# Kernel tuning notes

Measured on AMD Instinct MI355X. Metric: run time of the kernel, lower is better.

## Reference

```python
import jax, jax.numpy as jnp
import numpy as np

D_MODEL = 64
D_K = 64
D_V = 64
N_HEADS = 4
D_FF = 64
D_HALF = 32  # d_model / 2 in the sca_* MLPs


def _layer_norm(x, eps=1e-5):
    m = jnp.mean(x, axis=-1, keepdims=True)
    v = jnp.var(x, axis=-1, keepdims=True)
    return (x - m) / jnp.sqrt(v + eps)


def _sca(u, w1, w2):
    # nn.Sequential(Linear(64,32), ReLU, Linear(32,1)), no bias
    return jax.nn.relu(u @ w1) @ w2  # [B,1,1]


def setup_inputs() -> dict:
    key = jax.random.key(0)
    ks = jax.random.split(key, 20)
    B, L = 128, 512

    def lin(k, fan_in, fan_out):
        bound = 1.0 / np.sqrt(fan_in)
        return jax.random.uniform(k, (fan_in, fan_out), jnp.float32, -bound, bound)

    inp = {
        "input": jax.random.normal(ks[0], (B, L, D_MODEL), jnp.float32),
        "attn_mask": jax.random.bernoulli(ks[1], 0.1, (B, L, L)),
        "input_u": jax.random.normal(ks[2], (B, 1, D_MODEL), jnp.float32),
        "W_Q": lin(ks[3], D_MODEL, N_HEADS * D_K),
        "W_K": lin(ks[4], D_MODEL, N_HEADS * D_K),
        "W_V": lin(ks[5], D_MODEL, N_HEADS * D_V),
        "U_Q": lin(ks[6], D_MODEL, D_K),
        "U_K": lin(ks[7], D_MODEL, D_K),
        "U_V": lin(ks[8], D_MODEL, D_V),
        "sq1": lin(ks[9], D_MODEL, D_HALF),
        "sq2": lin(ks[10], D_HALF, 1),
        "sk1": lin(ks[11], D_MODEL, D_HALF),
        "sk2": lin(ks[12], D_HALF, 1),
        "sv1": lin(ks[13], D_MODEL, D_HALF),
        "sv2": lin(ks[14], D_HALF, 1),
        "fc": lin(ks[15], N_HEADS * D_V, D_MODEL),
        "ff1": lin(ks[16], D_MODEL, D_FF),
        "ff2": lin(ks[17], D_FF, D_MODEL),
    }
    return inp


def reference(input, attn_mask, input_u, W_Q, W_K, W_V, U_Q, U_K, U_V,
              sq1, sq2, sk1, sk2, sv1, sv2, fc, ff1, ff2):
    B, L, _ = input.shape
    scale = 1.0 / np.sqrt(D_K).astype(np.float32)

    # multi-head projections: [B, H, L, d]
    Q = (input @ W_Q).reshape(B, L, N_HEADS, D_K).transpose(0, 2, 1, 3)
    K = (input @ W_K).reshape(B, L, N_HEADS, D_K).transpose(0, 2, 1, 3)
    V = (input @ W_V).reshape(B, L, N_HEADS, D_V).transpose(0, 2, 1, 3)

    # per-batch scalar gates from input_u: [B,1,1]
    s_q = _sca(input_u, sq1, sq2)
    s_k = _sca(input_u, sk1, sk2)
    s_v = _sca(input_u, sv1, sv2)

    # single-head u projections, gated; broadcast over heads later
    u_Q = (input @ U_Q) * s_q  # [B, L, d_k]
    u_K = (input @ U_K) * s_k  # [B, L, d_k]
    u_V = (input @ U_V) * s_v  # [B, L, d_v]

    scores = jnp.einsum('bhqd,bhkd->bhqk', Q, K) * scale
    scores = scores + (jnp.einsum('bqd,bkd->bqk', u_Q, u_K) * scale)[:, None]
    scores = jnp.where(attn_mask[:, None], jnp.float32(-1e9), scores)
    attn = jax.nn.softmax(scores, axis=-1)  # [B, H, L, L]

    context = jnp.einsum('bhqk,bhkd->bhqd', attn, V + u_V[:, None])
    context = context.transpose(0, 2, 1, 3).reshape(B, L, N_HEADS * D_V)

    out = context @ fc  # dropout is identity in eval
    enc = _layer_norm(out + input)

    # position-wise FFN with residual + layernorm
    ffn = jax.nn.relu(enc @ ff1) @ ff2
    enc_outputs = _layer_norm(ffn + enc)
    return (enc_outputs, attn)
```

## Files before the change

### kernel.cpp

```cpp
#include <hip/hip_runtime.h>

typedef unsigned char  u8;
typedef unsigned short u16;
typedef unsigned int   u32;

typedef __attribute__((ext_vector_type(8))) short bf16x8;
typedef __attribute__((ext_vector_type(4))) float f32x4;

__device__ __forceinline__ u16 f2bf(float f) {
  union { float f; u32 u; } v; v.f = f;
  u32 u = v.u;
  u32 r = u + 0x7fffu + ((u >> 16) & 1u);
  return (u16)(r >> 16);
}
__device__ __forceinline__ float bf2f(u16 h) {
  union { u32 u; float f; } v; v.u = ((u32)h) << 16;
  return v.f;
}
__device__ __forceinline__ bf16x8 pack8(float4 a, float4 b) {
  bf16x8 r;
  r[0] = (short)f2bf(a.x); r[1] = (short)f2bf(a.y);
  r[2] = (short)f2bf(a.z); r[3] = (short)f2bf(a.w);
  r[4] = (short)f2bf(b.x); r[5] = (short)f2bf(b.y);
  r[6] = (short)f2bf(b.z); r[7] = (short)f2bf(b.w);
  return r;
}
__device__ __forceinline__ f32x4 mfma16(bf16x8 a, bf16x8 b, f32x4 c) {
  return __builtin_amdgcn_mfma_f32_16x16x32_bf16(a, b, c, 0, 0, 0);
}

__global__ void kflaginit(u32* flags) { flags[0] = 0; flags[1] = 0; }

__global__ void kscan(const u32* __restrict__ m, u32* __restrict__ flags) {
  int gid = blockIdx.x * 256 + threadIdx.x;
  const uint4* p = (const uint4*)m;
  u32 gt = 0, fp = 0;
#pragma unroll
  for (int i = 0; i < 4; ++i) {
    uint4 v = p[gid * 4 + i];
    gt |= (u32)((v.x > 1u) | (v.y > 1u) | (v.z > 1u) | (v.w > 1u));
    fp |= (u32)((v.x == 0x3F800000u) | (v.y == 0x3F800000u) |
                (v.z == 0x3F800000u) | (v.w == 0x3F800000u));
  }
  if (gt) flags[0] = 1;
  if (fp) flags[1] = 1;
}

__global__ void kconv(const void* __restrict__ m, const u32* __restrict__ flags,
                      u8* __restrict__ out) {
  int gid = blockIdx.x * 256 + threadIdx.x;
  u32 isf = flags[1], isb = flags[0];
  uchar4 o;
  if (isf) {
    float4 v = ((const float4*)m)[gid];
    o.x = v.x != 0.f; o.y = v.y != 0.f; o.z = v.z != 0.f; o.w = v.w != 0.f;
  } else if (isb) {
    uchar4 v = ((const uchar4*)m)[gid];
    o.x = v.x != 0; o.y = v.y != 0; o.z = v.z != 0; o.w = v.w != 0;
  } else {
    uint4 v = ((const uint4*)m)[gid];
    o.x = v.x != 0; o.y = v.y != 0; o.z = v.z != 0; o.w = v.w != 0;
  }
  ((uchar4*)out)[gid] = o;
}

__global__ void kgates(const float* __restrict__ iu,
                       const float* __restrict__ q1, const float* __restrict__ q2,
                       const float* __restrict__ k1, const float* __restrict__ k2,
                       const float* __restrict__ v1, const float* __restrict__ v2,
                       float* __restrict__ gates) {
  int b = blockIdx.x, t = threadIdx.x;
  __shared__ float u[64];
  u[t] = iu[b * 64 + t];
  __syncthreads();
  const float* w1[3] = {q1, k1, v1};
  const float* w2[3] = {q2, k2, v2};
#pragma unroll
  for (int m = 0; m < 3; ++m) {
    float p = 0.f;
    if (t < 32) {
      float h = 0.f;
      for (int i = 0; i < 64; ++i) h += u[i] * w1[m][i * 32 + t];
      h = fmaxf(h, 0.f);
      p = h * w2[m][t];
    }
    for (int off = 32; off >= 1; off >>= 1) p += __shfl_xor(p, off);
    if (t == 0) gates[m * 128 + b] = p;
  }
}

__launch_bounds__(256, 1)
__global__ void kproj_qk(const float* __restrict__ x,
                         const float* __restrict__ wq, const float* __restrict__ uq,
                         const float* __restrict__ wk, const float* __restrict__ uk,
                         const float* __restrict__ gates,
                         u16* __restrict__ qc, u16* __restrict__ qu,
                         u16* __restrict__ kc, u16* __restrict__ ku) {
  __shared__ u16 XT[64 * 136];
  __shared__ u16 WT[640 * 72];
  int b = blockIdx.x >> 3, l0 = (blockIdx.x & 7) * 64, t = threadIdx.x;
  {
    int tok = t >> 2, i0 = (t & 3) * 16;
    const float4* s = (const float4*)(x + ((size_t)(b * 512 + l0 + tok)) * 64 + i0);
    *(bf16x8*)&XT[tok * 136 + i0]     = pack8(s[0], s[1]);
    *(bf16x8*)&XT[tok * 136 + i0 + 8] = pack8(s[2], s[3]);
  }
  for (int i = 0; i < 64; ++i) { int e = t + i * 256; WT[(e & 255) * 72 + (e >> 8)] = (short)f2bf(wq[e]); }
  for (int i = 0; i < 16; ++i) { int e = t + i * 256; WT[(256 + (e & 63)) * 72 + (e >> 6)] = (short)f2bf(uq[e]); }
  for (int i = 0; i < 64; ++i) { int e = t + i * 256; WT[(320 + (e & 255)) * 72 + (e >> 8)] = (short)f2bf(wk[e]); }
  for (int i = 0; i < 16; ++i) { int e = t + i * 256; WT[(576 + (e & 63)) * 72 + (e >> 6)] = (short)f2bf(uk[e]); }
  __syncthreads();

  int w = t >> 6, lane = t & 63, lrow = lane & 15, lgrp = lane >> 4;
  bf16x8 af[4][2];
#pragma unroll
  for (int m = 0; m < 4; ++m)
#pragma unroll
    for (int fs = 0; fs < 2; ++fs)
      af[m][fs] = *(const bf16x8*)&XT[(m * 16 + lrow) * 136 + fs * 32 + lgrp * 8];

  float sq = gates[b], sk = gates[128 + b];
  const f32x4 fz = {0.f, 0.f, 0.f, 0.f};
#pragma unroll
  for (int part = 0; part < 2; ++part) {
    f32x4 acc[4][5];
#pragma unroll
    for (int m = 0; m < 4; ++m)
#pragma unroll
      for (int nt = 0; nt < 5; ++nt) acc[m][nt] = fz;
#pragma unroll
    for (int fs = 0; fs < 2; ++fs)
#pragma unroll
      for (int nt = 0; nt < 5; ++nt) {
        bf16x8 bf = *(const bf16x8*)&WT[(part * 320 + w * 80 + nt * 16 + lrow) * 72 + fs * 32 + lgrp * 8];
#pragma unroll
        for (int m = 0; m < 4; ++m)
          acc[m][nt] = mfma16(af[m][fs], bf, acc[m][nt]);
      }
    u16* dstC = part ? kc : qc;
    u16* dstU = part ? ku : qu;
    float presc = part ? 1.0f : 0.125f;
    float g = (part ? sk : sq) * presc;
#pragma unroll
    for (int nt = 0; nt < 5; ++nt) {
      int ncol = w * 80 + nt * 16 + lrow;
#pragma unroll
      for (int m = 0; m < 4; ++m)
#pragma unroll
        for (int j = 0; j < 4; ++j) {
          int l = l0 + m * 16 + lgrp * 4 + j;
          float v = acc[m][nt][j];
          if (ncol < 256) {
            dstC[(((size_t)(b * 4 + (ncol >> 6)) * 512) + l) * 64 + (ncol & 63)] = (short)f2bf(v * presc);
          } else {
            dstU[((size_t)b * 512 + l) * 64 + (ncol - 256)] = (short)f2bf(v * g);
          }
        }
    }
  }
}

__launch_bounds__(256, 1)
__global__ void kproj_v(const float* __restrict__ x,
                        const float* __restrict__ wv, const float* __restrict__ uv,
                        const float* __restrict__ gates, u16* __restrict__ vpt) {
  __shared__ u16 XT[64 * 136];
  __shared__ u16 WT[320 * 72];
  __shared__ float Vs[64 * 328];
  int b = blockIdx.x >> 3, l0 = (blockIdx.x & 7) * 64, t = threadIdx.x;
  {
    int tok = t >> 2, i0 = (t & 3) * 16;
    const float4* s = (const float4*)(x + ((size_t)(b * 512 + l0 + tok)) * 64 + i0);
    *(bf16x8*)&XT[tok * 136 + i0]     = pack8(s[0], s[1]);
    *(bf16x8*)&XT[tok * 136 + i0 + 8] = pack8(s[2], s[3]);
  }
  for (int i = 0; i < 64; ++i) { int e = t + i * 256; WT[(e & 255) * 72 + (e >> 8)] = (short)f2bf(wv[e]); }
  for (int i = 0; i < 16; ++i) { int e = t + i * 256; WT[(256 + (e & 63)) * 72 + (e >> 6)] = (short)f2bf(uv[e]); }
  __syncthreads();

  int w = t >> 6, lane = t & 63, lrow = lane & 15, lgrp = lane >> 4;
  bf16x8 af[4][2];
#pragma unroll
  for (int m = 0; m < 4; ++m)
#pragma unroll
    for (int fs = 0; fs < 2; ++fs)
      af[m][fs] = *(const bf16x8*)&XT[(m * 16 + lrow) * 136 + fs * 32 + lgrp * 8];

  const f32x4 fz = {0.f, 0.f, 0.f, 0.f};
  f32x4 acc[4][5];
#pragma unroll
  for (int m = 0; m < 4; ++m)
#pragma unroll
    for (int nt = 0; nt < 5; ++nt) acc[m][nt] = fz;
#pragma unroll
  for (int fs = 0; fs < 2; ++fs)
#pragma unroll
    for (int nt = 0; nt < 5; ++nt) {
      bf16x8 bf = *(const bf16x8*)&WT[(w * 80 + nt * 16 + lrow) * 72 + fs * 32 + lgrp * 8];
#pragma unroll
      for (int m = 0; m < 4; ++m)
        acc[m][nt] = mfma16(af[m][fs], bf, acc[m][nt]);
    }
#pragma unroll
  for (int nt = 0; nt < 5; ++nt)
#pragma unroll
    for (int m = 0; m < 4; ++m)
#pragma unroll
      for (int j = 0; j < 4; ++j)
        Vs[(m * 16 + lgrp * 4 + j) * 328 + w * 80 + nt * 16 + lrow] = acc[m][nt][j];
  __syncthreads();

  float sv = gates[256 + b];
#pragma unroll
  for (int p = 0; p < 4; ++p) {
    int hd = p * 64 + (t >> 2);
    int d = hd & 63;
    int tok0 = (t & 3) * 16;
    bf16x8 v0, v1;
#pragma unroll
    for (int i = 0; i < 8; ++i) {
      int tok = tok0 + i;
      v0[i] = (short)f2bf(Vs[tok * 328 + hd] + Vs[tok * 328 + 256 + d] * sv);
    }
#pragma unroll
    for (int i = 0; i < 8; ++i) {
      int tok = tok0 + 8 + i;
      v1[i] = (short)f2bf(Vs[tok * 328 + hd] + Vs[tok * 328 + 256 + d] * sv);
    }
    size_t base = (((size_t)(b * 4 + (hd >> 6)) * 64) + d) * 512 + l0 + tok0;
    *(bf16x8*)&vpt[base] = v0;
    *(bf16x8*)&vpt[base + 8] = v1;
  }
}

__launch_bounds__(512, 4)
__global__ void kattn(const u16* __restrict__ qc, const u16* __restrict__ qu,
                      const u16* __restrict__ kc, const u16* __restrict__ ku,
                      const u16* __restrict__ vpt, const u8* __restrict__ maskb,
                      float* __restrict__ aout, u16* __restrict__ ctx) {
  __shared__ char smem[53248];
  u16* QT = (u16*)smem;
  u16* KT = (u16*)(smem + 17408);
  float* SMm = (float*)(smem + 52224);
  float* SMl = (float*)(smem + 52736);
  u16* Vt = (u16*)smem;
  u16* Pl = (u16*)(smem + 17408);

  int bid = blockIdx.x;
  int logical = (bid & 7) * 512 + (bid >> 3);
  int b = logical >> 5;
  int r5 = logical & 31;
  int qt = r5 >> 2, hh = r5 & 3;
  int bh = b * 4 + hh;
  int q0 = qt * 64;

  int t = threadIdx.x, w = t >> 6, lane = t & 63, lrow = lane & 15, lgrp = lane >> 4;
  int qsub = w & 3, g = w >> 2, g64 = g * 64;

  {
    int tok = t >> 3, c0 = (t & 7) * 16;
    const u16* src = (c0 < 64)
      ? qc + ((size_t)bh * 512 + q0 + tok) * 64 + c0
      : qu + ((size_t)b  * 512 + q0 + tok) * 64 + (c0 - 64);
    *(bf16x8*)&QT[tok * 136 + c0]     = *(const bf16x8*)&src[0];
    *(bf16x8*)&QT[tok * 136 + c0 + 8] = *(const bf16x8*)&src[8];
  }

  const f32x4 fz = {0.f, 0.f, 0.f, 0.f};
  f32x4 acc[16];
#pragma unroll
  for (int i = 0; i < 16; ++i) acc[i] = fz;

#pragma unroll
  for (int kt = 0; kt < 4; ++kt) {
    __syncthreads();
    {
      int r = t >> 2, c0 = (t & 3) * 32;
      const u16* src = (c0 < 64)
        ? kc + ((size_t)bh * 512 + kt * 128 + r) * 64 + c0
        : ku + ((size_t)b  * 512 + kt * 128 + r) * 64 + (c0 - 64);
#pragma unroll
      for (int i = 0; i < 4; ++i)
        *(bf16x8*)&KT[r * 136 + c0 + i * 8] = *(const bf16x8*)&src[i * 8];
    }
    __syncthreads();
#pragma unroll
    for (int fs = 0; fs < 4; ++fs) {
      bf16x8 a = *(const bf16x8*)&QT[(qsub * 16 + lrow) * 136 + fs * 32 + lgrp * 8];
#pragma unroll
      for (int nt = 0; nt < 4; ++nt) {
        bf16x8 bf = *(const bf16x8*)&KT[(g64 + nt * 16 + lrow) * 136 + fs * 32 + lgrp * 8];
        acc[kt * 4 + nt] = mfma16(a, bf, acc[kt * 4 + nt]);
      }
    }
  }

  int qloc0 = qsub * 16 + lgrp * 4;
  const u8* mrow = maskb + ((size_t)b * 512 + q0 + qloc0) * 512;
  float mj[4] = {-3.0e38f, -3.0e38f, -3.0e38f, -3.0e38f};
#pragma unroll
  for (int i = 0; i < 16; ++i) {
    int kpos = (i >> 2) * 128 + g64 + (i & 3) * 16 + lrow;
#pragma unroll
    for (int j = 0; j < 4; ++j) {
      float s = acc[i][j];
      if (mrow[(size_t)j * 512 + kpos]) s = -1.0e9f;
      acc[i][j] = s;
      mj[j] = fmaxf(mj[j], s);
    }
  }
#pragma unroll
  for (int j = 0; j < 4; ++j) {
    mj[j] = fmaxf(mj[j], __shfl_xor(mj[j], 1));
    mj[j] = fmaxf(mj[j], __shfl_xor(mj[j], 2));
    mj[j] = fmaxf(mj[j], __shfl_xor(mj[j], 4));
    mj[j] = fmaxf(mj[j], __shfl_xor(mj[j], 8));
  }
  if (lrow == 0) {
#pragma unroll
    for (int j = 0; j < 4; ++j) SMm[g64 + qloc0 + j] = mj[j];
  }
  __syncthreads();
  float gm[4];
#pragma unroll
  for (int j = 0; j < 4; ++j) gm[j] = fmaxf(SMm[qloc0 + j], SMm[64 + qloc0 + j]);
  float lj[4] = {0.f, 0.f, 0.f, 0.f};
#pragma unroll
  for (int i = 0; i < 16; ++i)
#pragma unroll
    for (int j = 0; j < 4; ++j) {
      float p = __expf(acc[i][j] - gm[j]);
      acc[i][j] = p;
      lj[j] += p;
    }
#pragma unroll
  for (int j = 0; j < 4; ++j) {
    lj[j] += __shfl_xor(lj[j], 1);
    lj[j] += __shfl_xor(lj[j], 2);
    lj[j] += __shfl_xor(lj[j], 4);
    lj[j] += __shfl_xor(lj[j], 8);
  }
  if (lrow == 0) {
#pragma unroll
    for (int j = 0; j < 4; ++j) SMl[g64 + qloc0 + j] = lj[j];
  }
  __syncthreads();
  float inv[4];
#pragma unroll
  for (int j = 0; j < 4; ++j) inv[j] = 1.0f / (SMl[qloc0 + j] + SMl[64 + qloc0 + j]);

  size_t ab = ((size_t)bh * 512 + q0 + qloc0) * 512;
#pragma unroll
  for (int i = 0; i < 16; ++i) {
    int kpos = (i >> 2) * 128 + g64 + (i & 3) * 16 + lrow;
#pragma unroll
    for (int j = 0; j < 4; ++j) {
      float av = acc[i][j] * inv[j];
      acc[i][j] = av;
      aout[ab + (size_t)j * 512 + kpos] = av;
    }
  }

  f32x4 cacc[2] = {fz, fz};
#pragma unroll
  for (int c = 0; c < 4; ++c) {
    {
      int d = t >> 3, c0 = (t & 7) * 16;
      const u16* src = vpt + ((size_t)bh * 64 + d) * 512 + c * 128 + c0;
      *(bf16x8*)&Vt[d * 136 + c0]     = *(const bf16x8*)&src[0];
      *(bf16x8*)&Vt[d * 136 + c0 + 8] = *(const bf16x8*)&src[8];
    }
#pragma unroll
    for (int nt = 0; nt < 4; ++nt)
#pragma unroll
      for (int j = 0; j < 4; ++j)
        Pl[(qloc0 + j) * 136 + g64 + nt * 16 + lrow] = (short)f2bf(acc[c * 4 + nt][j]);
    __syncthreads();
#pragma unroll
    for (int ks = 0; ks < 4; ++ks) {
      bf16x8 a = *(const bf16x8*)&Pl[(qsub * 16 + lrow) * 136 + ks * 32 + lgrp * 8];
#pragma unroll
      for (int nt2 = 0; nt2 < 2; ++nt2) {
        bf16x8 bf = *(const bf16x8*)&Vt[(g * 32 + nt2 * 16 + lrow) * 136 + ks * 32 + lgrp * 8];
        cacc[nt2] = mfma16(a, bf, cacc[nt2]);
      }
    }
    __syncthreads();
  }
#pragma unroll
  for (int nt2 = 0; nt2 < 2; ++nt2)
#pragma unroll
    for (int j = 0; j < 4; ++j)
      ctx[((size_t)b * 512 + q0 + qloc0 + j) * 256 + hh * 64 + g * 32 + nt2 * 16 + lrow] =
          (short)f2bf(cacc[nt2][j]);
}

__launch_bounds__(256, 1)
__global__ void kffn(const u16* __restrict__ ctx, const float* __restrict__ x,
                     const float* __restrict__ fcw, const float* __restrict__ f1w,
                     const float* __restrict__ f2w, float* __restrict__ out) {
  __shared__ u16 CT[64 * 264];
  __shared__ u16 FCT[64 * 264];
  __shared__ u16 F1T[64 * 72];
  __shared__ u16 F2T[64 * 72];
  __shared__ float ENC[64 * 68];
  __shared__ u16 EBF[64 * 72];
  __shared__ u16 HBF[64 * 72];
  int b = blockIdx.x >> 3, l0 = (blockIdx.x & 7) * 64, t = threadIdx.x;
  {
    int tok = t >> 2, c0 = (t & 3) * 64;
    const u16* src = ctx + ((size_t)(b * 512 + l0 + tok)) * 256 + c0;
#pragma unroll
    for (int i = 0; i < 8; ++i)
      *(bf16x8*)&CT[tok * 264 + c0 + i * 8] = *(const bf16x8*)&src[i * 8];
  }
  for (int i = 0; i < 64; ++i) { int e = t + i * 256; FCT[(e & 63) * 264 + (e >> 6)] = (short)f2bf(fcw[e]); }
  for (int i = 0; i < 16; ++i) { int e = t + i * 256; F1T[(e & 63) * 72 + (e >> 6)] = (short)f2bf(f1w[e]); }
  for (int i = 0; i < 16; ++i) { int e = t + i * 256; F2T[(e & 63) * 72 + (e >> 6)] = (short)f2bf(f2w[e]); }
  __syncthreads();

  int w = t >> 6, lane = t & 63, lrow = lane & 15, lgrp = lane >> 4;
  int row = w * 16 + lgrp * 4;
  const f32x4 fz = {0.f, 0.f, 0.f, 0.f};

  f32x4 acc[4];
#pragma unroll
  for (int nt = 0; nt < 4; ++nt) acc[nt] = fz;
#pragma unroll
  for (int ks = 0; ks < 8; ++ks) {
    bf16x8 a = *(const bf16x8*)&CT[(w * 16 + lrow) * 264 + ks * 32 + lgrp * 8];
#pragma unroll
    for (int nt = 0; nt < 4; ++nt)
      acc[nt] = mfma16(a, *(const bf16x8*)&FCT[(nt * 16 + lrow) * 264 + ks * 32 + lgrp * 8], acc[nt]);
  }
  const float* xb = x + ((size_t)(b * 512 + l0)) * 64;
#pragma unroll
  for (int nt = 0; nt < 4; ++nt)
#pragma unroll
    for (int j = 0; j < 4; ++j)
      acc[nt][j] += xb[(row + j) * 64 + nt * 16 + lrow];

  float mean[4], rstd[4];
#pragma unroll
  for (int j = 0; j < 4; ++j) {
    float s = acc[0][j] + acc[1][j] + acc[2][j] + acc[3][j];
    s += __shfl_xor(s, 1); s += __shfl_xor(s, 2); s += __shfl_xor(s, 4); s += __shfl_xor(s, 8);
    mean[j] = s * 0.015625f;
  }
#pragma unroll
  for (int j = 0; j < 4; ++j) {
    float d0 = acc[0][j] - mean[j], d1 = acc[1][j] - mean[j];
    float d2 = acc[2][j] - mean[j], d3 = acc[3][j] - mean[j];
    float s = d0 * d0 + d1 * d1 + d2 * d2 + d3 * d3;
    s += __shfl_xor(s, 1); s += __shfl_xor(s, 2); s += __shfl_xor(s, 4); s += __shfl_xor(s, 8);
    rstd[j] = 1.0f / sqrtf(s * 0.015625f + 1e-5f);
  }
#pragma unroll
  for (int nt = 0; nt < 4; ++nt)
#pragma unroll
    for (int j = 0; j < 4; ++j) {
      float v = (acc[nt][j] - mean[j]) * rstd[j];
      ENC[(row + j) * 68 + nt * 16 + lrow] = v;
      EBF[(row + j) * 72 + nt * 16 + lrow] = (short)f2bf(v);
    }

  f32x4 h4[4];
#pragma unroll
  for (int nt = 0; nt < 4; ++nt) h4[nt] = fz;
#pragma unroll
  for (int ks = 0; ks < 2; ++ks) {
    bf16x8 a = *(const bf16x8*)&EBF[(w * 16 + lrow) * 72 + ks * 32 + lgrp * 8];
#pragma unroll
    for (int nt = 0; nt < 4; ++nt)
      h4[nt] = mfma16(a, *(const bf16x8*)&F1T[(nt * 16 + lrow) * 72 + ks * 32 + lgrp * 8], h4[nt]);
  }
#pragma unroll
  for (int nt = 0; nt < 4; ++nt)
#pragma unroll
    for (int j = 0; j < 4; ++j)
      HBF[(row + j) * 72 + nt * 16 + lrow] = (short)f2bf(fmaxf(h4[nt][j], 0.f));

  f32x4 o4[4];
#pragma unroll
  for (int nt = 0; nt < 4; ++nt) o4[nt] = fz;
#pragma unroll
  for (int ks = 0; ks < 2; ++ks) {
    bf16x8 a = *(const bf16x8*)&HBF[(w * 16 + lrow) * 72 + ks * 32 + lgrp * 8];
#pragma unroll
    for (int nt = 0; nt < 4; ++nt)
      o4[nt] = mfma16(a, *(const bf16x8*)&F2T[(nt * 16 + lrow) * 72 + ks * 32 + lgrp * 8], o4[nt]);
  }
#pragma unroll
  for (int nt = 0; nt < 4; ++nt)
#pragma unroll
    for (int j = 0; j < 4; ++j)
      o4[nt][j] += ENC[(row + j) * 68 + nt * 16 + lrow];

  float mean2[4], rstd2[4];
#pragma unroll
  for (int j = 0; j < 4; ++j) {
    float s = o4[0][j] + o4[1][j] + o4[2][j] + o4[3][j];
    s += __shfl_xor(s, 1); s += __shfl_xor(s, 2); s += __shfl_xor(s, 4); s += __shfl_xor(s, 8);
    mean2[j] = s * 0.015625f;
  }
#pragma unroll
  for (int j = 0; j < 4; ++j) {
    float d0 = o4[0][j] - mean2[j], d1 = o4[1][j] - mean2[j];
    float d2 = o4[2][j] - mean2[j], d3 = o4[3][j] - mean2[j];
    float s = d0 * d0 + d1 * d1 + d2 * d2 + d3 * d3;
    s += __shfl_xor(s, 1); s += __shfl_xor(s, 2); s += __shfl_xor(s, 4); s += __shfl_xor(s, 8);
    rstd2[j] = 1.0f / sqrtf(s * 0.015625f + 1e-5f);
  }
#pragma unroll
  for (int nt = 0; nt < 4; ++nt)
#pragma unroll
    for (int j = 0; j < 4; ++j)
      out[((size_t)(b * 512 + l0) + row + j) * 64 + nt * 16 + lrow] =
          (o4[nt][j] - mean2[j]) * rstd2[j];
}

extern "C" void kernel_launch(void* const* d_in, const int* in_sizes, int n_in,
                              void* d_out, int out_size, void* d_ws, size_t ws_size,
                              hipStream_t stream) {
  const float* x   = (const float*)d_in[0];
  const void*  msk = d_in[1];
  const float* iu  = (const float*)d_in[2];
  const float* wq  = (const float*)d_in[3];
  const float* wk  = (const float*)d_in[4];
  const float* wv  = (const float*)d_in[5];
  const float* uq  = (const float*)d_in[6];
  const float* uk  = (const float*)d_in[7];
  const float* uv  = (const float*)d_in[8];
  const float* q1  = (const float*)d_in[9];
  const float* q2  = (const float*)d_in[10];
  const float* k1  = (const float*)d_in[11];
  const float* k2  = (const float*)d_in[12];
  const float* v1  = (const float*)d_in[13];
  const float* v2  = (const float*)d_in[14];
  const float* fcw = (const float*)d_in[15];
  const float* f1w = (const float*)d_in[16];
  const float* f2w = (const float*)d_in[17];
  float* out = (float*)d_out;

  char* ws = (char*)d_ws;
  u32*   flags = (u32*)ws;
  float* gates = (float*)(ws + 64);
  u16* qc  = (u16*)(ws + 4096);
  u16* qu  = (u16*)(ws + 33558528);
  u16* kc  = (u16*)(ws + 41947136);
  u16* ku  = (u16*)(ws + 75501568);
  u16* vpt = (u16*)(ws + 83890176);
  u8*  mb  = (u8*) (ws + 117444608);
  u16* ctx = (u16*)(ws + 150999040);

  kflaginit<<<dim3(1), dim3(1), 0, stream>>>(flags);
  kscan<<<dim3(1024), dim3(256), 0, stream>>>((const u32*)msk, flags);
  kconv<<<dim3(32768), dim3(256), 0, stream>>>(msk, flags, mb);
  kgates<<<dim3(128), dim3(64), 0, stream>>>(iu, q1, q2, k1, k2, v1, v2, gates);
  kproj_qk<<<dim3(1024), dim3(256), 0, stream>>>(x, wq, uq, wk, uk, gates, qc, qu, kc, ku);
  kproj_v<<<dim3(1024), dim3(256), 0, stream>>>(x, wv, uv, gates, vpt);
  kattn<<<dim3(4096), dim3(512), 0, stream>>>(qc, qu, kc, ku, vpt, mb, out + 4194304, ctx);
  kffn<<<dim3(1024), dim3(256), 0, stream>>>(ctx, x, fcw, f1w, f2w, out);
}
```

Baseline: 463.7 us.

## Pre-transpose weights once and restructure attention loads

Adds a prep kernel that converts and transposes every weight matrix to bf16 once and computes the gates, replacing the per-block weight staging in LDS inside the projection and FFN kernels. Those kernels now read weight fragments straight from global memory and use launch bounds of two blocks per CU. The attention kernel keeps Q fragments in registers, register-prefetches the next K tile while the current one is consumed, loads V fragments directly from global memory, and fuses the probability normalization and output store into the PV loop. This removes redundant per-block conversion work and LDS pressure, at the cost of more uncached-looking global fragment loads and higher register use.

```diff
diff --git a/kernel.cpp b/kernel.cpp
--- a/kernel.cpp
+++ b/kernel.cpp
@@ -12,10 +12,6 @@
   u32 u = v.u;
   u32 r = u + 0x7fffu + ((u >> 16) & 1u);
   return (u16)(r >> 16);
-}
-__device__ __forceinline__ float bf2f(u16 h) {
-  union { u32 u; float f; } v; v.u = ((u32)h) << 16;
-  return v.f;
 }
 __device__ __forceinline__ bf16x8 pack8(float4 a, float4 b) {
   bf16x8 r;
@@ -64,40 +60,79 @@
   ((uchar4*)out)[gid] = o;
 }
 
-__global__ void kgates(const float* __restrict__ iu,
-                       const float* __restrict__ q1, const float* __restrict__ q2,
-                       const float* __restrict__ k1, const float* __restrict__ k2,
-                       const float* __restrict__ v1, const float* __restrict__ v2,
-                       float* __restrict__ gates) {
-  int b = blockIdx.x, t = threadIdx.x;
-  __shared__ float u[64];
-  u[t] = iu[b * 64 + t];
-  __syncthreads();
-  const float* w1[3] = {q1, k1, v1};
-  const float* w2[3] = {q2, k2, v2};
-#pragma unroll
-  for (int m = 0; m < 3; ++m) {
-    float p = 0.f;
-    if (t < 32) {
-      float h = 0.f;
-      for (int i = 0; i < 64; ++i) h += u[i] * w1[m][i * 32 + t];
-      h = fmaxf(h, 0.f);
-      p = h * w2[m][t];
-    }
-    for (int off = 32; off >= 1; off >>= 1) p += __shfl_xor(p, off);
-    if (t == 0) gates[m * 128 + b] = p;
-  }
-}
-
-__launch_bounds__(256, 1)
+__global__ void kprep(const float* __restrict__ wq, const float* __restrict__ wk,
+                      const float* __restrict__ wv, const float* __restrict__ uq,
+                      const float* __restrict__ uk, const float* __restrict__ uv,
+                      const float* __restrict__ fc, const float* __restrict__ f1,
+                      const float* __restrict__ f2, const float* __restrict__ iu,
+                      const float* __restrict__ q1, const float* __restrict__ q2,
+                      const float* __restrict__ k1, const float* __restrict__ k2,
+                      const float* __restrict__ v1, const float* __restrict__ v2,
+                      u16* __restrict__ wqT, u16* __restrict__ wkT, u16* __restrict__ wvT,
+                      u16* __restrict__ uqT, u16* __restrict__ ukT, u16* __restrict__ uvT,
+                      u16* __restrict__ fcT, u16* __restrict__ f1T, u16* __restrict__ f2T,
+                      float* __restrict__ gates) {
+  int bid = blockIdx.x, t = threadIdx.x;
+  if (bid < 3) {
+    const float* src = bid == 0 ? wq : bid == 1 ? wk : wv;
+    u16* dst = bid == 0 ? wqT : bid == 1 ? wkT : wvT;
+    for (int i = 0; i < 64; ++i) {
+      int e = t + i * 256; int n = e & 255, k = e >> 8;
+      dst[n * 64 + k] = f2bf(src[k * 256 + n]);
+    }
+  } else if (bid < 6) {
+    const float* src = bid == 3 ? uq : bid == 4 ? uk : uv;
+    u16* dst = bid == 3 ? uqT : bid == 4 ? ukT : uvT;
+    for (int i = 0; i < 16; ++i) {
+      int e = t + i * 256; int n = e & 63, k = e >> 6;
+      dst[n * 64 + k] = f2bf(src[k * 64 + n]);
+    }
+  } else if (bid == 6) {
+    for (int i = 0; i < 64; ++i) {
+      int e = t + i * 256; int n = e & 63, k = e >> 6;
+      fcT[n * 256 + k] = f2bf(fc[k * 64 + n]);
+    }
+  } else if (bid == 7) {
+    for (int i = 0; i < 16; ++i) {
+      int e = t + i * 256; int n = e & 63, k = e >> 6;
+      f1T[n * 64 + k] = f2bf(f1[k * 64 + n]);
+    }
+  } else if (bid == 8) {
+    for (int i = 0; i < 16; ++i) {
+      int e = t + i * 256; int n = e & 63, k = e >> 6;
+      f2T[n * 64 + k] = f2bf(f2[k * 64 + n]);
+    }
+  } else {
+    int b = bid - 9;
+    __shared__ float u[64];
+    if (t < 64) u[t] = iu[b * 64 + t];
+    __syncthreads();
+    if (t < 64) {
+      const float* w1[3] = {q1, k1, v1};
+      const float* w2[3] = {q2, k2, v2};
+#pragma unroll
+      for (int m = 0; m < 3; ++m) {
+        float p = 0.f;
+        if (t < 32) {
+          float h = 0.f;
+          for (int i = 0; i < 64; ++i) h += u[i] * w1[m][i * 32 + t];
+          p = fmaxf(h, 0.f) * w2[m][t];
+        }
+        for (int off = 32; off >= 1; off >>= 1) p += __shfl_xor(p, off);
+        if (t == 0) gates[m * 128 + b] = p;
+      }
+    }
+  }
+}
+
+__launch_bounds__(256, 2)
 __global__ void kproj_qk(const float* __restrict__ x,
-                         const float* __restrict__ wq, const float* __restrict__ uq,
-                         const float* __restrict__ wk, const float* __restrict__ uk,
+                         const u16* __restrict__ wqT, const u16* __restrict__ uqT,
+                         const u16* __restrict__ wkT, const u16* __restrict__ ukT,
                          const float* __restrict__ gates,
                          u16* __restrict__ qc, u16* __restrict__ qu,
                          u16* __restrict__ kc, u16* __restrict__ ku) {
   __shared__ u16 XT[64 * 136];
-  __shared__ u16 WT[640 * 72];
   int b = blockIdx.x >> 3, l0 = (blockIdx.x & 7) * 64, t = threadIdx.x;
   {
     int tok = t >> 2, i0 = (t & 3) * 16;
@@ -105,10 +140,6 @@
     *(bf16x8*)&XT[tok * 136 + i0]     = pack8(s[0], s[1]);
     *(bf16x8*)&XT[tok * 136 + i0 + 8] = pack8(s[2], s[3]);
   }
-  for (int i = 0; i < 64; ++i) { int e = t + i * 256; WT[(e & 255) * 72 + (e >> 8)] = (short)f2bf(wq[e]); }
-  for (int i = 0; i < 16; ++i) { int e = t + i * 256; WT[(256 + (e & 63)) * 72 + (e >> 6)] = (short)f2bf(uq[e]); }
-  for (int i = 0; i < 64; ++i) { int e = t + i * 256; WT[(320 + (e & 255)) * 72 + (e >> 8)] = (short)f2bf(wk[e]); }
-  for (int i = 0; i < 16; ++i) { int e = t + i * 256; WT[(576 + (e & 63)) * 72 + (e >> 6)] = (short)f2bf(uk[e]); }
   __syncthreads();
 
   int w = t >> 6, lane = t & 63, lrow = lane & 15, lgrp = lane >> 4;
@@ -123,6 +154,8 @@
   const f32x4 fz = {0.f, 0.f, 0.f, 0.f};
 #pragma unroll
   for (int part = 0; part < 2; ++part) {
+    const u16* WT = part ? wkT : wqT;
+    const u16* UT = part ? ukT : uqT;
     f32x4 acc[4][5];
 #pragma unroll
     for (int m = 0; m < 4; ++m)
@@ -132,7 +165,9 @@
     for (int fs = 0; fs < 2; ++fs)
 #pragma unroll
       for (int nt = 0; nt < 5; ++nt) {
-        bf16x8 bf = *(const bf16x8*)&WT[(part * 320 + w * 80 + nt * 16 + lrow) * 72 + fs * 32 + lgrp * 8];
+        const u16* src = (nt < 4) ? WT + (w * 64 + nt * 16 + lrow) * 64
+                                  : UT + (w * 16 + lrow) * 64;
+        bf16x8 bf = *(const bf16x8*)(src + fs * 32 + lgrp * 8);
 #pragma unroll
         for (int m = 0; m < 4; ++m)
           acc[m][nt] = mfma16(af[m][fs], bf, acc[m][nt]);
@@ -140,33 +175,33 @@
     u16* dstC = part ? kc : qc;
     u16* dstU = part ? ku : qu;
     float presc = part ? 1.0f : 0.125f;
-    float g = (part ? sk : sq) * presc;
+    float gg = (part ? sk : sq) * presc;
 #pragma unroll
     for (int nt = 0; nt < 5; ++nt) {
-      int ncol = w * 80 + nt * 16 + lrow;
 #pragma unroll
       for (int m = 0; m < 4; ++m)
 #pragma unroll
         for (int j = 0; j < 4; ++j) {
           int l = l0 + m * 16 + lgrp * 4 + j;
           float v = acc[m][nt][j];
-          if (ncol < 256) {
+          if (nt < 4) {
+            int ncol = w * 64 + nt * 16 + lrow;
             dstC[(((size_t)(b * 4 + (ncol >> 6)) * 512) + l) * 64 + (ncol & 63)] = (short)f2bf(v * presc);
           } else {
-            dstU[((size_t)b * 512 + l) * 64 + (ncol - 256)] = (short)f2bf(v * g);
+            int uc = w * 16 + lrow;
+            dstU[((size_t)b * 512 + l) * 64 + uc] = (short)f2bf(v * gg);
           }
         }
     }
   }
 }
 
-__launch_bounds__(256, 1)
+__launch_bounds__(256, 2)
 __global__ void kproj_v(const float* __restrict__ x,
-                        const float* __restrict__ wv, const float* __restrict__ uv,
+                        const u16* __restrict__ wvT, const u16* __restrict__ uvT,
                         const float* __restrict__ gates, u16* __restrict__ vpt) {
   __shared__ u16 XT[64 * 136];
-  __shared__ u16 WT[320 * 72];
-  __shared__ float Vs[64 * 328];
+  __shared__ float Vs[64 * 329];
   int b = blockIdx.x >> 3, l0 = (blockIdx.x & 7) * 64, t = threadIdx.x;
   {
     int tok = t >> 2, i0 = (t & 3) * 16;
@@ -174,8 +209,6 @@
     *(bf16x8*)&XT[tok * 136 + i0]     = pack8(s[0], s[1]);
     *(bf16x8*)&XT[tok * 136 + i0 + 8] = pack8(s[2], s[3]);
   }
-  for (int i = 0; i < 64; ++i) { int e = t + i * 256; WT[(e & 255) * 72 + (e >> 8)] = (short)f2bf(wv[e]); }
-  for (int i = 0; i < 16; ++i) { int e = t + i * 256; WT[(256 + (e & 63)) * 72 + (e >> 6)] = (short)f2bf(uv[e]); }
   __syncthreads();
 
   int w = t >> 6, lane = t & 63, lrow = lane & 15, lgrp = lane >> 4;
@@ -196,7 +229,9 @@
   for (int fs = 0; fs < 2; ++fs)
 #pragma unroll
     for (int nt = 0; nt < 5; ++nt) {
-      bf16x8 bf = *(const bf16x8*)&WT[(w * 80 + nt * 16 + lrow) * 72 + fs * 32 + lgrp * 8];
+      const u16* src = (nt < 4) ? wvT + (w * 64 + nt * 16 + lrow) * 64
+                                : uvT + (w * 16 + lrow) * 64;
+      bf16x8 bf = *(const bf16x8*)(src + fs * 32 + lgrp * 8);
 #pragma unroll
       for (int m = 0; m < 4; ++m)
         acc[m][nt] = mfma16(af[m][fs], bf, acc[m][nt]);
@@ -206,8 +241,11 @@
 #pragma unroll
     for (int m = 0; m < 4; ++m)
 #pragma unroll
-      for (int j = 0; j < 4; ++j)
-        Vs[(m * 16 + lgrp * 4 + j) * 328 + w * 80 + nt * 16 + lrow] = acc[m][nt][j];
+      for (int j = 0; j < 4; ++j) {
+        int tok = m * 16 + lgrp * 4 + j;
+        int col = (nt < 4) ? (w * 64 + nt * 16 + lrow) : (256 + w * 16 + lrow);
+        Vs[tok * 329 + col] = acc[m][nt][j];
+      }
   __syncthreads();
 
   float sv = gates[256 + b];
@@ -220,12 +258,12 @@
 #pragma unroll
     for (int i = 0; i < 8; ++i) {
       int tok = tok0 + i;
-      v0[i] = (short)f2bf(Vs[tok * 328 + hd] + Vs[tok * 328 + 256 + d] * sv);
+      v0[i] = (short)f2bf(Vs[tok * 329 + hd] + Vs[tok * 329 + 256 + d] * sv);
     }
 #pragma unroll
     for (int i = 0; i < 8; ++i) {
       int tok = tok0 + 8 + i;
-      v1[i] = (short)f2bf(Vs[tok * 328 + hd] + Vs[tok * 328 + 256 + d] * sv);
+      v1[i] = (short)f2bf(Vs[tok * 329 + hd] + Vs[tok * 329 + 256 + d] * sv);
     }
     size_t base = (((size_t)(b * 4 + (hd >> 6)) * 64) + d) * 512 + l0 + tok0;
     *(bf16x8*)&vpt[base] = v0;
@@ -239,12 +277,10 @@
                       const u16* __restrict__ vpt, const u8* __restrict__ maskb,
                       float* __restrict__ aout, u16* __restrict__ ctx) {
   __shared__ char smem[53248];
-  u16* QT = (u16*)smem;
-  u16* KT = (u16*)(smem + 17408);
+  u16* KT = (u16*)smem;
+  u16* Pl = (u16*)(smem + 34816);
   float* SMm = (float*)(smem + 52224);
   float* SMl = (float*)(smem + 52736);
-  u16* Vt = (u16*)smem;
-  u16* Pl = (u16*)(smem + 17408);
 
   int bid = blockIdx.x;
   int logical = (bid & 7) * 512 + (bid >> 3);
@@ -256,16 +292,33 @@
 
   int t = threadIdx.x, w = t >> 6, lane = t & 63, lrow = lane & 15, lgrp = lane >> 4;
   int qsub = w & 3, g = w >> 2, g64 = g * 64;
-
+  int qloc0 = qsub * 16 + lgrp * 4;
+
+  bf16x8 qf[4];
   {
-    int tok = t >> 3, c0 = (t & 7) * 16;
-    const u16* src = (c0 < 64)
-      ? qc + ((size_t)bh * 512 + q0 + tok) * 64 + c0
-      : qu + ((size_t)b  * 512 + q0 + tok) * 64 + (c0 - 64);
-    *(bf16x8*)&QT[tok * 136 + c0]     = *(const bf16x8*)&src[0];
-    *(bf16x8*)&QT[tok * 136 + c0 + 8] = *(const bf16x8*)&src[8];
-  }
-
+    const u16* qrow = qc + ((size_t)bh * 512 + q0 + qsub * 16 + lrow) * 64;
+    const u16* urow = qu + ((size_t)b  * 512 + q0 + qsub * 16 + lrow) * 64;
+    qf[0] = *(const bf16x8*)(qrow + lgrp * 8);
+    qf[1] = *(const bf16x8*)(qrow + 32 + lgrp * 8);
+    qf[2] = *(const bf16x8*)(urow + lgrp * 8);
+    qf[3] = *(const bf16x8*)(urow + 32 + lgrp * 8);
+  }
+
+  int r = t >> 2;
+  uint4 kreg[4];
+#define LDK(kt)                                                                   \
+  {                                                                               \
+    _Pragma("unroll")                                                             \
+    for (int i = 0; i < 4; ++i) {                                                 \
+      int c = (t & 3) * 4 + i;                                                    \
+      const u16* src = (c < 8)                                                    \
+        ? kc + ((size_t)bh * 512 + (kt) * 128 + r) * 64 + c * 8                   \
+        : ku + ((size_t)b  * 512 + (kt) * 128 + r) * 64 + (c - 8) * 8;            \
+      kreg[i] = *(const uint4*)src;                                               \
+    }                                                                             \
+  }
+
+  LDK(0);
   const f32x4 fz = {0.f, 0.f, 0.f, 0.f};
   f32x4 acc[16];
 #pragma unroll
@@ -274,28 +327,20 @@
 #pragma unroll
   for (int kt = 0; kt < 4; ++kt) {
     __syncthreads();
-    {
-      int r = t >> 2, c0 = (t & 3) * 32;
-      const u16* src = (c0 < 64)
-        ? kc + ((size_t)bh * 512 + kt * 128 + r) * 64 + c0
-        : ku + ((size_t)b  * 512 + kt * 128 + r) * 64 + (c0 - 64);
-#pragma unroll
-      for (int i = 0; i < 4; ++i)
-        *(bf16x8*)&KT[r * 136 + c0 + i * 8] = *(const bf16x8*)&src[i * 8];
-    }
+#pragma unroll
+    for (int i = 0; i < 4; ++i)
+      *(uint4*)&KT[r * 136 + ((t & 3) * 4 + i) * 8] = kreg[i];
+    if (kt < 3) LDK(kt + 1);
     __syncthreads();
 #pragma unroll
-    for (int fs = 0; fs < 4; ++fs) {
-      bf16x8 a = *(const bf16x8*)&QT[(qsub * 16 + lrow) * 136 + fs * 32 + lgrp * 8];
+    for (int fs = 0; fs < 4; ++fs)
 #pragma unroll
       for (int nt = 0; nt < 4; ++nt) {
         bf16x8 bf = *(const bf16x8*)&KT[(g64 + nt * 16 + lrow) * 136 + fs * 32 + lgrp * 8];
-        acc[kt * 4 + nt] = mfma16(a, bf, acc[kt * 4 + nt]);
+        acc[kt * 4 + nt] = mfma16(qf[fs], bf, acc[kt * 4 + nt]);
       }
-    }
-  }
-
-  int qloc0 = qsub * 16 + lgrp * 4;
+  }
+
   const u8* mrow = maskb + ((size_t)b * 512 + q0 + qloc0) * 512;
   float mj[4] = {-3.0e38f, -3.0e38f, -3.0e38f, -3.0e38f};
 #pragma unroll
@@ -350,42 +395,33 @@
   for (int j = 0; j < 4; ++j) inv[j] = 1.0f / (SMl[qloc0 + j] + SMl[64 + qloc0 + j]);
 
   size_t ab = ((size_t)bh * 512 + q0 + qloc0) * 512;
-#pragma unroll
-  for (int i = 0; i < 16; ++i) {
-    int kpos = (i >> 2) * 128 + g64 + (i & 3) * 16 + lrow;
-#pragma unroll
-    for (int j = 0; j < 4; ++j) {
-      float av = acc[i][j] * inv[j];
-      acc[i][j] = av;
-      aout[ab + (size_t)j * 512 + kpos] = av;
-    }
-  }
-
   f32x4 cacc[2] = {fz, fz};
 #pragma unroll
   for (int c = 0; c < 4; ++c) {
-    {
-      int d = t >> 3, c0 = (t & 7) * 16;
-      const u16* src = vpt + ((size_t)bh * 64 + d) * 512 + c * 128 + c0;
-      *(bf16x8*)&Vt[d * 136 + c0]     = *(const bf16x8*)&src[0];
-      *(bf16x8*)&Vt[d * 136 + c0 + 8] = *(const bf16x8*)&src[8];
-    }
+    bf16x8 vf[4][2];
+#pragma unroll
+    for (int ks = 0; ks < 4; ++ks)
+#pragma unroll
+      for (int nt2 = 0; nt2 < 2; ++nt2)
+        vf[ks][nt2] = *(const bf16x8*)(vpt + ((size_t)bh * 64 + g * 32 + nt2 * 16 + lrow) * 512
+                                       + c * 128 + ks * 32 + lgrp * 8);
+    if (c) __syncthreads();
 #pragma unroll
     for (int nt = 0; nt < 4; ++nt)
 #pragma unroll
-      for (int j = 0; j < 4; ++j)
-        Pl[(qloc0 + j) * 136 + g64 + nt * 16 + lrow] = (short)f2bf(acc[c * 4 + nt][j]);
+      for (int j = 0; j < 4; ++j) {
+        float val = acc[c * 4 + nt][j] * inv[j];
+        int kin = g64 + nt * 16 + lrow;
+        aout[ab + (size_t)j * 512 + c * 128 + kin] = val;
+        Pl[(qloc0 + j) * 136 + kin] = (short)f2bf(val);
+      }
     __syncthreads();
 #pragma unroll
     for (int ks = 0; ks < 4; ++ks) {
       bf16x8 a = *(const bf16x8*)&Pl[(qsub * 16 + lrow) * 136 + ks * 32 + lgrp * 8];
-#pragma unroll
-      for (int nt2 = 0; nt2 < 2; ++nt2) {
-        bf16x8 bf = *(const bf16x8*)&Vt[(g * 32 + nt2 * 16 + lrow) * 136 + ks * 32 + lgrp * 8];
-        cacc[nt2] = mfma16(a, bf, cacc[nt2]);
-      }
-    }
-    __syncthreads();
+      cacc[0] = mfma16(a, vf[ks][0], cacc[0]);
+      cacc[1] = mfma16(a, vf[ks][1], cacc[1]);
+    }
   }
 #pragma unroll
   for (int nt2 = 0; nt2 < 2; ++nt2)
@@ -395,30 +431,14 @@
           (short)f2bf(cacc[nt2][j]);
 }
 
-__launch_bounds__(256, 1)
+__launch_bounds__(256, 2)
 __global__ void kffn(const u16* __restrict__ ctx, const float* __restrict__ x,
-                     const float* __restrict__ fcw, const float* __restrict__ f1w,
-                     const float* __restrict__ f2w, float* __restrict__ out) {
-  __shared__ u16 CT[64 * 264];
-  __shared__ u16 FCT[64 * 264];
-  __shared__ u16 F1T[64 * 72];
-  __shared__ u16 F2T[64 * 72];
+                     const u16* __restrict__ fcT, const u16* __restrict__ f1T,
+                     const u16* __restrict__ f2T, float* __restrict__ out) {
   __shared__ float ENC[64 * 68];
   __shared__ u16 EBF[64 * 72];
   __shared__ u16 HBF[64 * 72];
   int b = blockIdx.x >> 3, l0 = (blockIdx.x & 7) * 64, t = threadIdx.x;
-  {
-    int tok = t >> 2, c0 = (t & 3) * 64;
-    const u16* src = ctx + ((size_t)(b * 512 + l0 + tok)) * 256 + c0;
-#pragma unroll
-    for (int i = 0; i < 8; ++i)
-      *(bf16x8*)&CT[tok * 264 + c0 + i * 8] = *(const bf16x8*)&src[i * 8];
-  }
-  for (int i = 0; i < 64; ++i) { int e = t + i * 256; FCT[(e & 63) * 264 + (e >> 6)] = (short)f2bf(fcw[e]); }
-  for (int i = 0; i < 16; ++i) { int e = t + i * 256; F1T[(e & 63) * 72 + (e >> 6)] = (short)f2bf(f1w[e]); }
-  for (int i = 0; i < 16; ++i) { int e = t + i * 256; F2T[(e & 63) * 72 + (e >> 6)] = (short)f2bf(f2w[e]); }
-  __syncthreads();
-
   int w = t >> 6, lane = t & 63, lrow = lane & 15, lgrp = lane >> 4;
   int row = w * 16 + lgrp * 4;
   const f32x4 fz = {0.f, 0.f, 0.f, 0.f};
@@ -428,10 +448,12 @@
   for (int nt = 0; nt < 4; ++nt) acc[nt] = fz;
 #pragma unroll
   for (int ks = 0; ks < 8; ++ks) {
-    bf16x8 a = *(const bf16x8*)&CT[(w * 16 + lrow) * 264 + ks * 32 + lgrp * 8];
-#pragma unroll
-    for (int nt = 0; nt < 4; ++nt)
-      acc[nt] = mfma16(a, *(const bf16x8*)&FCT[(nt * 16 + lrow) * 264 + ks * 32 + lgrp * 8], acc[nt]);
+    bf16x8 a = *(const bf16x8*)(ctx + ((size_t)(b * 512 + l0 + w * 16 + lrow)) * 256 + ks * 32 + lgrp * 8);
+#pragma unroll
+    for (int nt = 0; nt < 4; ++nt) {
+      bf16x8 bf = *(const bf16x8*)(fcT + (nt * 16 + lrow) * 256 + ks * 32 + lgrp * 8);
+      acc[nt] = mfma16(a, bf, acc[nt]);
+    }
   }
   const float* xb = x + ((size_t)(b * 512 + l0)) * 64;
 #pragma unroll
@@ -471,8 +493,10 @@
   for (int ks = 0; ks < 2; ++ks) {
     bf16x8 a = *(const bf16x8*)&EBF[(w * 16 + lrow) * 72 + ks * 32 + lgrp * 8];
 #pragma unroll
-    for (int nt = 0; nt < 4; ++nt)
-      h4[nt] = mfma16(a, *(const bf16x8*)&F1T[(nt * 16 + lrow) * 72 + ks * 32 + lgrp * 8], h4[nt]);
+    for (int nt = 0; nt < 4; ++nt) {
+      bf16x8 bf = *(const bf16x8*)(f1T + (nt * 16 + lrow) * 64 + ks * 32 + lgrp * 8);
+      h4[nt] = mfma16(a, bf, h4[nt]);
+    }
   }
 #pragma unroll
   for (int nt = 0; nt < 4; ++nt)
@@ -487,8 +511,10 @@
   for (int ks = 0; ks < 2; ++ks) {
     bf16x8 a = *(const bf16x8*)&HBF[(w * 16 + lrow) * 72 + ks * 32 + lgrp * 8];
 #pragma unroll
-    for (int nt = 0; nt < 4; ++nt)
-      o4[nt] = mfma16(a, *(const bf16x8*)&F2T[(nt * 16 + lrow) * 72 + ks * 32 + lgrp * 8], o4[nt]);
+    for (int nt = 0; nt < 4; ++nt) {
+      bf16x8 bf = *(const bf16x8*)(f2T + (nt * 16 + lrow) * 64 + ks * 32 + lgrp * 8);
+      o4[nt] = mfma16(a, bf, o4[nt]);
+    }
   }
 #pragma unroll
   for (int nt = 0; nt < 4; ++nt)
@@ -545,20 +571,31 @@
   char* ws = (char*)d_ws;
   u32*   flags = (u32*)ws;
   float* gates = (float*)(ws + 64);
-  u16* qc  = (u16*)(ws + 4096);
-  u16* qu  = (u16*)(ws + 33558528);
-  u16* kc  = (u16*)(ws + 41947136);
-  u16* ku  = (u16*)(ws + 75501568);
-  u16* vpt = (u16*)(ws + 83890176);
-  u8*  mb  = (u8*) (ws + 117444608);
-  u16* ctx = (u16*)(ws + 150999040);
+  u16* wqT = (u16*)(ws + 4096);
+  u16* wkT = (u16*)(ws + 36864);
+  u16* wvT = (u16*)(ws + 69632);
+  u16* uqT = (u16*)(ws + 102400);
+  u16* ukT = (u16*)(ws + 110592);
+  u16* uvT = (u16*)(ws + 118784);
+  u16* fcT = (u16*)(ws + 126976);
+  u16* f1T = (u16*)(ws + 159744);
+  u16* f2T = (u16*)(ws + 167936);
+  u16* qc  = (u16*)(ws + 180224);
+  u16* qu  = (u16*)(ws + 33734656);
+  u16* kc  = (u16*)(ws + 42123264);
+  u16* ku  = (u16*)(ws + 75677696);
+  u16* vpt = (u16*)(ws + 84066304);
+  u8*  mb  = (u8*) (ws + 117620736);
+  u16* ctx = (u16*)(ws + 151175168);
 
   kflaginit<<<dim3(1), dim3(1), 0, stream>>>(flags);
   kscan<<<dim3(1024), dim3(256), 0, stream>>>((const u32*)msk, flags);
   kconv<<<dim3(32768), dim3(256), 0, stream>>>(msk, flags, mb);
-  kgates<<<dim3(128), dim3(64), 0, stream>>>(iu, q1, q2, k1, k2, v1, v2, gates);
-  kproj_qk<<<dim3(1024), dim3(256), 0, stream>>>(x, wq, uq, wk, uk, gates, qc, qu, kc, ku);
-  kproj_v<<<dim3(1024), dim3(256), 0, stream>>>(x, wv, uv, gates, vpt);
+  kprep<<<dim3(137), dim3(256), 0, stream>>>(wq, wk, wv, uq, uk, uv, fcw, f1w, f2w,
+                                             iu, q1, q2, k1, k2, v1, v2,
+                                             wqT, wkT, wvT, uqT, ukT, uvT, fcT, f1T, f2T, gates);
+  kproj_qk<<<dim3(1024), dim3(256), 0, stream>>>(x, wqT, uqT, wkT, ukT, gates, qc, qu, kc, ku);
+  kproj_v<<<dim3(1024), dim3(256), 0, stream>>>(x, wvT, uvT, gates, vpt);
   kattn<<<dim3(4096), dim3(512), 0, stream>>>(qc, qu, kc, ku, vpt, mb, out + 4194304, ctx);
-  kffn<<<dim3(1024), dim3(256), 0, stream>>>(ctx, x, fcw, f1w, f2w, out);
-}
+  kffn<<<dim3(1024), dim3(256), 0, stream>>>(ctx, x, fcT, f1T, f2T, out);
+}
```

Result: slower. 638.1 us (+37.6%).
